# Kernel optimization log

Measured on AMD Instinct MI355X. Metric: run time of the kernel, lower is better.

## Reference

```python
import jax, jax.numpy as jnp
import numpy as np

D_MODEL = 1024; D_STATE = 128; EXPAND = 2; HEADDIM = 64
D_INNER = EXPAND * D_MODEL; NHEADS = D_INNER // HEADDIM; PF = 2  # param_factor for complex
BATCH = 2; SEQ = 2048
DT_MIN = 0.001; DT_MAX = 0.1


def setup_inputs() -> dict:
    key = jax.random.key(0)
    k = jax.random.split(key, 10)
    u = jax.random.normal(k[0], (BATCH, SEQ, D_MODEL), jnp.float32)
    in_proj_w = jax.random.normal(k[1], (2 * D_INNER, D_MODEL), jnp.float32) * (D_MODEL ** -0.5)
    dt_projs_weight = jax.random.normal(k[2], (NHEADS, D_INNER), jnp.float32) * 0.02
    dt_projs_bias = (jax.random.uniform(k[3], (NHEADS,), jnp.float32)
                     * (np.log(DT_MAX) - np.log(DT_MIN)) + np.log(DT_MIN)).astype(jnp.float32)
    x_proj_w = jax.random.normal(k[4], (NHEADS * (1 + 2 * D_STATE * PF), D_INNER), jnp.float32) * (D_INNER ** -0.5)
    A = jnp.stack([-jax.random.uniform(k[5], (NHEADS, D_STATE), dtype=jnp.float32),
                   jax.random.normal(k[6], (NHEADS, D_STATE), jnp.float32) * 0.1], axis=-1)  # (H,N,2)
    D = jnp.ones((NHEADS,), jnp.float32)
    norm_B_w = jnp.ones((2 * D_STATE,), jnp.float32)
    norm_C_w = jnp.ones((2 * D_STATE,), jnp.float32)
    out_proj_w = jax.random.normal(k[7], (D_MODEL, D_INNER), jnp.float32) * (D_INNER ** -0.5)
    return {"u": u, "in_proj_w": in_proj_w, "dt_projs_weight": dt_projs_weight,
            "dt_projs_bias": dt_projs_bias, "x_proj_w": x_proj_w, "A": A, "D": D,
            "norm_B_w": norm_B_w, "norm_C_w": norm_C_w, "out_proj_w": out_proj_w}


def _rms_norm(x, w, eps=1e-6):
    return x * jax.lax.rsqrt(jnp.mean(x * x, axis=-1, keepdims=True) + eps) * w


def reference(u, in_proj_w, dt_projs_weight, dt_projs_bias, x_proj_w, A, D,
              norm_B_w, norm_C_w, out_proj_w):
    Bsz, L, _ = u.shape
    xz = u @ in_proj_w.T                        # (B,L,2*d_inner)
    x, z = jnp.split(xz, 2, axis=-1)
    x = jax.nn.silu(x)                          # (B,L,d_inner)
    dt = jax.nn.softplus(x @ dt_projs_weight.T + dt_projs_bias)  # (B,L,H)

    BCp = (x @ x_proj_w.T).reshape(Bsz, L, NHEADS, -1)
    BC = BCp[..., :2 * D_STATE * PF].reshape(Bsz, L, NHEADS, 2, D_STATE, PF)
    Bn = _rms_norm(BC[..., 0, :, :].reshape(Bsz, L, NHEADS, D_STATE * PF), norm_B_w)
    Cn = _rms_norm(BC[..., 1, :, :].reshape(Bsz, L, NHEADS, D_STATE * PF), norm_C_w)
    Bn = Bn.reshape(Bsz, L, NHEADS, D_STATE, PF)
    Cn = Cn.reshape(Bsz, L, NHEADS, D_STATE, PF)
    Bc = jax.lax.complex(Bn[..., 0], Bn[..., 1])  # (B,L,H,N) complex64
    Cc = jax.lax.complex(Cn[..., 0], Cn[..., 1])
    Ac = jax.lax.complex(A[..., 0], A[..., 1])    # (H,N) complex64

    xh = x.reshape(Bsz, L, NHEADS, HEADDIM)
    x_sum = xh.sum(axis=-1)                       # (B,L,H) -- kernel sums x_t over headdim
    zt = Ac[None, None] * (0.5 * dt)[..., None]   # (B,L,H,N) complex: A*dt/2
    den = 1.0 - zt
    abar = (1.0 + zt) / den                       # bilinear (Tustin) discretization
    u_in = Bc * ((dt * x_sum)[..., None] / den)   # Bbar * sum(x_t)

    def step(h, inp):
        a, b = inp
        h = a * h + b
        return h, h

    h0 = jnp.zeros((Bsz, NHEADS, D_STATE), jnp.complex64)
    _, hs = jax.lax.scan(step, h0, (jnp.swapaxes(abar, 0, 1), jnp.swapaxes(u_in, 0, 1)))
    hs = jnp.swapaxes(hs, 0, 1)                   # (B,L,H,N)
    y_red = jnp.real(Cc * hs).sum(axis=-1)        # (B,L,H), Re(C*h) reduced over state
    y = (xh * (y_red + D)[..., None]).reshape(Bsz, L, D_INNER)
    y = y * jax.nn.silu(z)
    return y @ out_proj_w.T
```

## Files before the change

### kernel.cpp

```cpp
#include <hip/hip_runtime.h>

#define BATCH   2
#define SEQ     2048
#define DMODEL  1024
#define DINNER  2048
#define NHEADS  32
#define HEADDIM 64
#define DSTATE  128
#define BLTOT   (BATCH * SEQ)
#define NCHUNK  32
#define CHUNK   64

#define OFF_UB   0ull
#define OFF_WXZ  8388608ull
#define OFF_WBC  16777216ull
#define OFF_WOUT 83886080ull
#define OFF_XB   88080384ull
#define OFF_YB   104857600ull
#define OFF_BC   121634816ull
#define OFF_SZ   255852544ull
#define OFF_DT   272629760ull
#define OFF_XS   273154048ull
#define OFF_YR   273678336ull
#define OFF_CA   274202624ull
#define OFF_CS   276299776ull
#define OFF_HI   278396928ull
#define OFF_SS   280494080ull
#define OFF_P0   281542656ull
#define OFF_P1   298319872ull

typedef __attribute__((ext_vector_type(8))) short bf16x8;
typedef __attribute__((ext_vector_type(4))) float f32x4;

__device__ __forceinline__ float b2f(unsigned short u) {
    return __uint_as_float(((unsigned)u) << 16);
}
__device__ __forceinline__ unsigned short f2b(float f) {
    unsigned x = __float_as_uint(f);
    unsigned r = (x + 0x7fffu + ((x >> 16) & 1u)) >> 16;
    return (unsigned short)r;
}
__device__ __forceinline__ float silu_f(float v) {
    return v / (1.0f + __expf(-v));
}
__device__ __forceinline__ float softplus_f(float v) {
    return (v > 20.0f) ? v : log1pf(__expf(v));
}

__device__ __forceinline__ void gload_lds16(const void* g, void* l) {
    __builtin_amdgcn_global_load_lds(
        (const __attribute__((address_space(1))) unsigned int*)g,
        (__attribute__((address_space(3))) unsigned int*)l, 16, 0, 0);
}

__global__ __launch_bounds__(256) void conv_all_kernel(
    const float* __restrict__ u, const float* __restrict__ ipw,
    const float* __restrict__ opw, const float* __restrict__ xpw,
    unsigned short* __restrict__ u_b, unsigned short* __restrict__ w_xz,
    unsigned short* __restrict__ w_out, unsigned short* __restrict__ w_bc) {
    long idx = (long)blockIdx.x * 256 + threadIdx.x;
    if (idx >= 2621440L) {
        long e = (idx - 2621440L) * 4;
        long c = e >> 11, k = e & 2047;
        const float* s = xpw + ((c >> 9) * 513 + (c & 511)) * 2048 + k;
        float4 v = *(const float4*)s;
        ushort4 o = {f2b(v.x), f2b(v.y), f2b(v.z), f2b(v.w)};
        *(ushort4*)&w_bc[e] = o;
        return;
    }
    const float* src;
    unsigned short* dst;
    long i;
    if (idx < 1048576L)      { src = u;   dst = u_b;   i = idx; }
    else if (idx < 2097152L) { src = ipw; dst = w_xz;  i = idx - 1048576L; }
    else                     { src = opw; dst = w_out; i = idx - 2097152L; }
    float4 v = *(const float4*)&src[i * 4];
    ushort4 o = {f2b(v.x), f2b(v.y), f2b(v.z), f2b(v.w)};
    *(ushort4*)&dst[i * 4] = o;
}

template <int KTOT, int KLEN, int MODE>
__device__ __forceinline__ void gemm_body(
    const unsigned short* __restrict__ A, const unsigned short* __restrict__ B,
    void* __restrict__ C0, void* __restrict__ C1, float* __restrict__ C2,
    int N, int koff) {
    __shared__ short ldsA[128 * 32];
    __shared__ short ldsB[128 * 32];
    int tid = threadIdx.x;
    int row0 = blockIdx.y * 128, col0 = blockIdx.x * 128;
    int lane = tid & 63, wave = tid >> 6;
    int wrow = (wave >> 1) * 64, wcol = (wave & 1) * 64;
    int m = lane & 15, quad = lane >> 4;

    f32x4 acc[4][4];
#pragma unroll
    for (int i = 0; i < 4; ++i)
#pragma unroll
        for (int j = 0; j < 4; ++j) acc[i][j] = (f32x4){0.f, 0.f, 0.f, 0.f};

    int r = tid >> 2, c8 = (tid & 3) * 8;
    const unsigned short* Ag = A + (size_t)(row0 + r) * KTOT + koff + c8;
    const unsigned short* Bg = B + (size_t)(col0 + r) * KTOT + koff + c8;
    short* la = ldsA + tid * 8;
    short* lb = ldsB + tid * 8;

    for (int k0 = 0; k0 < KLEN; k0 += 32) {
        gload_lds16(Ag + k0, la);
        gload_lds16(Ag + (size_t)64 * KTOT + k0, la + 2048);
        gload_lds16(Bg + k0, lb);
        gload_lds16(Bg + (size_t)64 * KTOT + k0, lb + 2048);
        __syncthreads();
        bf16x8 af[4], bfr[4];
#pragma unroll
        for (int i = 0; i < 4; ++i)
            af[i] = *(const bf16x8*)&ldsA[(wrow + i * 16 + m) * 32 + quad * 8];
#pragma unroll
        for (int j = 0; j < 4; ++j)
            bfr[j] = *(const bf16x8*)&ldsB[(wcol + j * 16 + m) * 32 + quad * 8];
#pragma unroll
        for (int i = 0; i < 4; ++i)
#pragma unroll
            for (int j = 0; j < 4; ++j)
                acc[i][j] = __builtin_amdgcn_mfma_f32_16x16x32_bf16(
                    af[i], bfr[j], acc[i][j], 0, 0, 0);
        __syncthreads();
    }

    if (MODE == 1) {
        bool isx = (col0 < DINNER);
        if (isx) {
            int head = (col0 + wcol) >> 6;
            float ssum[4][4];
#pragma unroll
            for (int i = 0; i < 4; ++i)
#pragma unroll
                for (int reg = 0; reg < 4; ++reg) ssum[i][reg] = 0.f;
#pragma unroll
            for (int i = 0; i < 4; ++i)
#pragma unroll
                for (int reg = 0; reg < 4; ++reg) {
                    int row = row0 + wrow + i * 16 + quad * 4 + reg;
#pragma unroll
                    for (int j = 0; j < 4; ++j) {
                        int col = col0 + wcol + j * 16 + m;
                        float s = silu_f(acc[i][j][reg]);
                        ((unsigned short*)C0)[(size_t)row * DINNER + col] = f2b(s);
                        ssum[i][reg] += s;
                    }
                }
#pragma unroll
            for (int i = 0; i < 4; ++i)
#pragma unroll
                for (int reg = 0; reg < 4; ++reg) {
                    float s = ssum[i][reg];
                    s += __shfl_xor(s, 1);
                    s += __shfl_xor(s, 2);
                    s += __shfl_xor(s, 4);
                    s += __shfl_xor(s, 8);
                    if (m == 0) {
                        int row = row0 + wrow + i * 16 + quad * 4 + reg;
                        C2[(size_t)row * NHEADS + head] = s;
                    }
                }
        } else {
#pragma unroll
            for (int i = 0; i < 4; ++i)
#pragma unroll
                for (int reg = 0; reg < 4; ++reg) {
                    int row = row0 + wrow + i * 16 + quad * 4 + reg;
#pragma unroll
                    for (int j = 0; j < 4; ++j) {
                        int col = col0 + wcol + j * 16 + m - DINNER;
                        float s = silu_f(acc[i][j][reg]);
                        ((unsigned short*)C1)[(size_t)row * DINNER + col] = f2b(s);
                    }
                }
        }
    } else if (MODE == 2) {
        int hH = (col0 + wcol) >> 9;
        int w0 = (col0 + wcol) & 511;
#pragma unroll
        for (int i = 0; i < 4; ++i)
#pragma unroll
            for (int reg = 0; reg < 4; ++reg) {
                int row = row0 + wrow + i * 16 + quad * 4 + reg;
                unsigned short* dst =
                    (unsigned short*)C0 + ((size_t)hH * BLTOT + row) * 512 + w0;
#pragma unroll
                for (int j = 0; j < 4; ++j)
                    dst[j * 16 + m] = f2b(acc[i][j][reg]);
            }
    } else {
#pragma unroll
        for (int i = 0; i < 4; ++i)
#pragma unroll
            for (int reg = 0; reg < 4; ++reg) {
                int row = row0 + wrow + i * 16 + quad * 4 + reg;
#pragma unroll
                for (int j = 0; j < 4; ++j) {
                    int col = col0 + wcol + j * 16 + m;
                    ((float*)C0)[(size_t)row * N + col] = acc[i][j][reg];
                }
            }
    }
}

__global__ __launch_bounds__(256) void gemm_xz_kernel(
    const unsigned short* __restrict__ A, const unsigned short* __restrict__ B,
    void* C0, void* C1, float* C2) {
    gemm_body<1024, 1024, 1>(A, B, C0, C1, C2, 4096, 0);
}
__global__ __launch_bounds__(256) void gemm_bc_kernel(
    const unsigned short* __restrict__ A, const unsigned short* __restrict__ B,
    void* C0) {
    gemm_body<2048, 2048, 2>(A, B, C0, nullptr, nullptr, 16384, 0);
}
__global__ __launch_bounds__(256) void gemm_out_kernel(
    const unsigned short* __restrict__ A, const unsigned short* __restrict__ B,
    float* P0, float* P1) {
    float* dst = blockIdx.z ? P1 : P0;
    gemm_body<2048, 1024, 0>(A, B, dst, nullptr, nullptr, 1024,
                             blockIdx.z * 1024);
}

__global__ __launch_bounds__(256) void yout_reduce_kernel(
    const float* __restrict__ p0, const float* __restrict__ p1,
    float* __restrict__ out) {
    int i = (blockIdx.x * 256 + threadIdx.x) * 4;
    float4 a = *(const float4*)&p0[i];
    float4 b = *(const float4*)&p1[i];
    float4 o = {a.x + b.x, a.y + b.y, a.z + b.z, a.w + b.w};
    *(float4*)&out[i] = o;
}

__global__ __launch_bounds__(256) void dt_kernel(
    const unsigned short* __restrict__ x, const float* __restrict__ dtw,
    const float* __restrict__ dtb, float* __restrict__ dt) {
    __shared__ float xs[8][132];
    __shared__ float ws[32][132];
    int r0 = blockIdx.x * 8;
    int t = threadIdx.x;
    int lrow = t >> 5, lc4 = (t & 31) * 4;
    int lh = t >> 3, lc16 = (t & 7) * 16;
    int row = t >> 5, h = t & 31;
    float acc = 0.f;

    for (int kc = 0; kc < DINNER; kc += 128) {
        ushort4 a = *(const ushort4*)&x[(size_t)(r0 + lrow) * DINNER + kc + lc4];
        xs[lrow][lc4 + 0] = b2f(a.x); xs[lrow][lc4 + 1] = b2f(a.y);
        xs[lrow][lc4 + 2] = b2f(a.z); xs[lrow][lc4 + 3] = b2f(a.w);
#pragma unroll
        for (int q = 0; q < 4; ++q) {
            float4 w = *(const float4*)&dtw[(size_t)lh * DINNER + kc + lc16 + q * 4];
            *(float4*)&ws[lh][lc16 + q * 4] = w;
        }
        __syncthreads();
#pragma unroll
        for (int k = 0; k < 128; k += 4) {
            float4 xv = *(const float4*)&xs[row][k];
            float4 wv = *(const float4*)&ws[h][k];
            acc += xv.x * wv.x + xv.y * wv.y + xv.z * wv.z + xv.w * wv.w;
        }
        __syncthreads();
    }
    dt[(size_t)(r0 + row) * NHEADS + h] = softplus_f(acc + dtb[h]);
}

__global__ __launch_bounds__(256) void ss_kernel(
    const unsigned short* __restrict__ bct, float* __restrict__ ss) {
    int wgid = blockIdx.x * 4 + (threadIdx.x >> 6);
    int lane = threadIdx.x & 63;
    const unsigned short* p = bct + (size_t)wgid * 512 + lane * 8;
    ushort4 a = *(const ushort4*)p;
    ushort4 b = *(const ushort4*)(p + 4);
    float f0 = b2f(a.x), f1 = b2f(a.y), f2 = b2f(a.z), f3 = b2f(a.w);
    float f4 = b2f(b.x), f5 = b2f(b.y), f6 = b2f(b.z), f7 = b2f(b.w);
    float s = f0 * f0 + f1 * f1 + f2 * f2 + f3 * f3 +
              f4 * f4 + f5 * f5 + f6 * f6 + f7 * f7;
    s += __shfl_xor(s, 1);
    s += __shfl_xor(s, 2);
    s += __shfl_xor(s, 4);
    s += __shfl_xor(s, 8);
    s += __shfl_xor(s, 16);
    if ((lane & 31) == 0) ss[(size_t)wgid * 2 + (lane >> 5)] = s;
}

__device__ __forceinline__ void coefs(
    float ar, float ai, float dtv, float xsv, float Br, float Bi,
    float& abr, float& abi, float& ur, float& ui) {
    float hd = 0.5f * dtv;
    float ztr = ar * hd, zti = ai * hd;
    float denr = 1.0f - ztr;
    float s2 = 1.0f / (denr * denr + zti * zti);
    float invr = denr * s2, invi = zti * s2;
    float opr = 1.0f + ztr;
    abr = opr * invr - zti * invi;
    abi = opr * invi + zti * invr;
    float coef = dtv * xsv;
    float cr = coef * invr, ci = coef * invi;
    ur = Br * cr - Bi * ci;
    ui = Br * ci + Bi * cr;
}

__global__ __launch_bounds__(64) void scan_pass1(
    const unsigned short* __restrict__ bct, const float* __restrict__ dt,
    const float* __restrict__ xsum, const float* __restrict__ A,
    const float* __restrict__ wB, const float* __restrict__ ss,
    float2* __restrict__ cA, float2* __restrict__ cS) {
    int blk = blockIdx.x;
    int bh = blk >> 5, c = blk & (NCHUNK - 1);
    int b = bh >> 5, h = bh & 31;
    int t = threadIdx.x;
    float4 av = *(const float4*)&A[(h * DSTATE + 2 * t) * 2];
    float4 wv = *(const float4*)&wB[4 * t];
    int l0 = c * CHUNK;
    size_t rbase = (size_t)h * BLTOT + b * SEQ + l0;
    const unsigned short* base = bct + rbase * 512;
    const float* ssp = ss + rbase * 2;
    const float* dtp = dt + (b * SEQ + l0) * NHEADS + h;
    const float* xsp = xsum + (b * SEQ + l0) * NHEADS + h;

    float pr0 = 1.f, pi0 = 0.f, sr0 = 0.f, si0 = 0.f;
    float pr1 = 1.f, pi1 = 0.f, sr1 = 0.f, si1 = 0.f;
    for (int l = 0; l < CHUNK; ++l) {
        uint2 bw = *(const uint2*)&base[(size_t)l * 512 + 4 * t];
        float scale = rsqrtf(ssp[l * 2] * (1.0f / 256.0f) + 1e-6f);
        float Br0 = b2f((unsigned short)(bw.x & 0xffff)) * scale * wv.x;
        float Bi0 = b2f((unsigned short)(bw.x >> 16)) * scale * wv.y;
        float Br1 = b2f((unsigned short)(bw.y & 0xffff)) * scale * wv.z;
        float Bi1 = b2f((unsigned short)(bw.y >> 16)) * scale * wv.w;
        float dtv = dtp[l * NHEADS], xsv = xsp[l * NHEADS];
        float abr, abi, ur, ui;
        coefs(av.x, av.y, dtv, xsv, Br0, Bi0, abr, abi, ur, ui);
        float ns = abr * sr0 - abi * si0 + ur;
        float nsi = abr * si0 + abi * sr0 + ui;
        sr0 = ns; si0 = nsi;
        float np = abr * pr0 - abi * pi0;
        float npi = abr * pi0 + abi * pr0;
        pr0 = np; pi0 = npi;
        coefs(av.z, av.w, dtv, xsv, Br1, Bi1, abr, abi, ur, ui);
        ns = abr * sr1 - abi * si1 + ur;
        nsi = abr * si1 + abi * sr1 + ui;
        sr1 = ns; si1 = nsi;
        np = abr * pr1 - abi * pi1;
        npi = abr * pi1 + abi * pr1;
        pr1 = np; pi1 = npi;
    }
    size_t idx = ((size_t)bh * NCHUNK + c) * DSTATE + 2 * t;
    *(float4*)&cA[idx] = (float4){pr0, pi0, pr1, pi1};
    *(float4*)&cS[idx] = (float4){sr0, si0, sr1, si1};
}

__global__ __launch_bounds__(128) void scan_fixup(
    const float2* __restrict__ cA, const float2* __restrict__ cS,
    float2* __restrict__ hin) {
    int bh = blockIdx.x;
    int n = threadIdx.x;
    float hr = 0.f, hi = 0.f;
    for (int c = 0; c < NCHUNK; ++c) {
        size_t idx = ((size_t)bh * NCHUNK + c) * DSTATE + n;
        hin[idx] = {hr, hi};
        float2 a = cA[idx];
        float2 s = cS[idx];
        float nhr = a.x * hr - a.y * hi + s.x;
        float nhi = a.x * hi + a.y * hr + s.y;
        hr = nhr; hi = nhi;
    }
}

__global__ __launch_bounds__(64) void scan_pass2(
    const unsigned short* __restrict__ bct, const float* __restrict__ dt,
    const float* __restrict__ xsum, const float* __restrict__ A,
    const float* __restrict__ wB, const float* __restrict__ wC,
    const float* __restrict__ ss, const float2* __restrict__ hin,
    float* __restrict__ yredp) {
    int blk = blockIdx.x;
    int bh = blk >> 5, c = blk & (NCHUNK - 1);
    int b = bh >> 5, h = bh & 31;
    int t = threadIdx.x;
    float4 av = *(const float4*)&A[(h * DSTATE + 2 * t) * 2];
    float4 wbv = *(const float4*)&wB[4 * t];
    float4 wcv = *(const float4*)&wC[4 * t];
    int l0 = c * CHUNK;
    size_t rbase = (size_t)h * BLTOT + b * SEQ + l0;
    const unsigned short* base = bct + rbase * 512;
    const float* ssp = ss + rbase * 2;
    const float* dtp = dt + (b * SEQ + l0) * NHEADS + h;
    const float* xsp = xsum + (b * SEQ + l0) * NHEADS + h;
    float* yp = yredp + (size_t)(b * SEQ + l0) * NHEADS + h;

    float4 h0v = *(const float4*)&hin[((size_t)bh * NCHUNK + c) * DSTATE + 2 * t];
    float hr0 = h0v.x, hi0 = h0v.y, hr1 = h0v.z, hi1 = h0v.w;

    for (int l = 0; l < CHUNK; ++l) {
        uint2 bw = *(const uint2*)&base[(size_t)l * 512 + 4 * t];
        uint2 cw = *(const uint2*)&base[(size_t)l * 512 + 256 + 4 * t];
        float sB = rsqrtf(ssp[l * 2 + 0] * (1.0f / 256.0f) + 1e-6f);
        float sC = rsqrtf(ssp[l * 2 + 1] * (1.0f / 256.0f) + 1e-6f);
        float Br0 = b2f((unsigned short)(bw.x & 0xffff)) * sB * wbv.x;
        float Bi0 = b2f((unsigned short)(bw.x >> 16)) * sB * wbv.y;
        float Br1 = b2f((unsigned short)(bw.y & 0xffff)) * sB * wbv.z;
        float Bi1 = b2f((unsigned short)(bw.y >> 16)) * sB * wbv.w;
        float Cr0 = b2f((unsigned short)(cw.x & 0xffff)) * sC * wcv.x;
        float Ci0 = b2f((unsigned short)(cw.x >> 16)) * sC * wcv.y;
        float Cr1 = b2f((unsigned short)(cw.y & 0xffff)) * sC * wcv.z;
        float Ci1 = b2f((unsigned short)(cw.y >> 16)) * sC * wcv.w;
        float dtv = dtp[l * NHEADS], xsv = xsp[l * NHEADS];
        float abr, abi, ur, ui;
        coefs(av.x, av.y, dtv, xsv, Br0, Bi0, abr, abi, ur, ui);
        float nhr = abr * hr0 - abi * hi0 + ur;
        float nhi = abr * hi0 + abi * hr0 + ui;
        hr0 = nhr; hi0 = nhi;
        coefs(av.z, av.w, dtv, xsv, Br1, Bi1, abr, abi, ur, ui);
        nhr = abr * hr1 - abi * hi1 + ur;
        nhi = abr * hi1 + abi * hr1 + ui;
        hr1 = nhr; hi1 = nhi;
        float y = Cr0 * hr0 - Ci0 * hi0 + Cr1 * hr1 - Ci1 * hi1;
#pragma unroll
        for (int off = 1; off < 64; off <<= 1) y += __shfl_xor(y, off);
        if (t == 0) yp[(size_t)l * NHEADS] = y;
    }
}

__global__ __launch_bounds__(256) void yfuse_kernel(
    const unsigned short* __restrict__ x, const unsigned short* __restrict__ sz,
    const float* __restrict__ yredp, const float* __restrict__ Dv,
    unsigned short* __restrict__ y) {
    int i = (blockIdx.x * 256 + threadIdx.x) * 4;
    int r = i >> 11;
    int k = i & (DINNER - 1);
    int h = k >> 6;
    float yr = yredp[(size_t)r * NHEADS + h] + Dv[h];
    ushort4 xv = *(const ushort4*)&x[i];
    ushort4 zv = *(const ushort4*)&sz[i];
    ushort4 o = {f2b(b2f(xv.x) * yr * b2f(zv.x)),
                 f2b(b2f(xv.y) * yr * b2f(zv.y)),
                 f2b(b2f(xv.z) * yr * b2f(zv.z)),
                 f2b(b2f(xv.w) * yr * b2f(zv.w))};
    *(ushort4*)&y[i] = o;
}

extern "C" void kernel_launch(void* const* d_in, const int* in_sizes, int n_in,
                              void* d_out, int out_size, void* d_ws, size_t ws_size,
                              hipStream_t stream) {
    const float* u   = (const float*)d_in[0];
    const float* ipw = (const float*)d_in[1];
    const float* dtw = (const float*)d_in[2];
    const float* dtb = (const float*)d_in[3];
    const float* xpw = (const float*)d_in[4];
    const float* A   = (const float*)d_in[5];
    const float* Dv  = (const float*)d_in[6];
    const float* wB  = (const float*)d_in[7];
    const float* wC  = (const float*)d_in[8];
    const float* opw = (const float*)d_in[9];
    float* out = (float*)d_out;
    char* ws = (char*)d_ws;

    unsigned short* u_b   = (unsigned short*)(ws + OFF_UB);
    unsigned short* w_xz  = (unsigned short*)(ws + OFF_WXZ);
    unsigned short* w_bc  = (unsigned short*)(ws + OFF_WBC);
    unsigned short* w_out = (unsigned short*)(ws + OFF_WOUT);
    unsigned short* x_b   = (unsigned short*)(ws + OFF_XB);
    unsigned short* y_b   = (unsigned short*)(ws + OFF_YB);
    unsigned short* bct   = (unsigned short*)(ws + OFF_BC);
    unsigned short* sz    = (unsigned short*)(ws + OFF_SZ);
    float* dt    = (float*)(ws + OFF_DT);
    float* xsum  = (float*)(ws + OFF_XS);
    float* yredp = (float*)(ws + OFF_YR);
    float2* cA   = (float2*)(ws + OFF_CA);
    float2* cS   = (float2*)(ws + OFF_CS);
    float2* hin  = (float2*)(ws + OFF_HI);
    float* ssbuf = (float*)(ws + OFF_SS);
    float* p0    = (float*)(ws + OFF_P0);
    float* p1    = (float*)(ws + OFF_P1);

    conv_all_kernel<<<43008, 256, 0, stream>>>(u, ipw, opw, xpw,
                                               u_b, w_xz, w_out, w_bc);

    gemm_xz_kernel<<<dim3(32, 32), 256, 0, stream>>>(u_b, w_xz, x_b, sz, xsum);
    dt_kernel<<<BLTOT / 8, 256, 0, stream>>>(x_b, dtw, dtb, dt);
    gemm_bc_kernel<<<dim3(128, 32), 256, 0, stream>>>(x_b, w_bc, bct);
    ss_kernel<<<NHEADS * BLTOT / 4, 256, 0, stream>>>(bct, ssbuf);

    scan_pass1<<<BATCH * NHEADS * NCHUNK, 64, 0, stream>>>(
        bct, dt, xsum, A, wB, ssbuf, cA, cS);
    scan_fixup<<<BATCH * NHEADS, 128, 0, stream>>>(cA, cS, hin);
    scan_pass2<<<BATCH * NHEADS * NCHUNK, 64, 0, stream>>>(
        bct, dt, xsum, A, wB, wC, ssbuf, hin, yredp);

    yfuse_kernel<<<BLTOT * DINNER / 4 / 256, 256, 0, stream>>>(
        x_b, sz, yredp, Dv, y_b);
    gemm_out_kernel<<<dim3(8, 32, 2), 256, 0, stream>>>(y_b, w_out, p0, p1);
    yout_reduce_kernel<<<BLTOT * DMODEL / 4 / 256, 256, 0, stream>>>(p0, p1, out);
}
```

Before: 832.5 us.

## Fuse y gating into scan pass2, deepen GEMM K-step, precompute rms scales

Removes the separate yfuse kernel: scan_pass2 now multiplies x, the reduced y plus D, and silu(z) directly, writing bf16 y per lane, which drops the yredp round trip and one launch. The shared GEMM body now stages 64 K elements per LDS load instead of 32, halving the number of barriers per tile while doubling LDS use. The RMS-norm rsqrt is moved into ss_kernel so the scan passes read the finished scale instead of recomputing it. The fused epilogue issues 2-byte stores per lane with a stride of one row per step, which coalesces less well than the old vectorized kernel.

```diff
diff --git a/kernel.cpp b/kernel.cpp
--- a/kernel.cpp
+++ b/kernel.cpp
@@ -21,7 +21,6 @@
 #define OFF_SZ   255852544ull
 #define OFF_DT   272629760ull
 #define OFF_XS   273154048ull
-#define OFF_YR   273678336ull
 #define OFF_CA   274202624ull
 #define OFF_CS   276299776ull
 #define OFF_HI   278396928ull
@@ -84,8 +83,8 @@
     const unsigned short* __restrict__ A, const unsigned short* __restrict__ B,
     void* __restrict__ C0, void* __restrict__ C1, float* __restrict__ C2,
     int N, int koff) {
-    __shared__ short ldsA[128 * 32];
-    __shared__ short ldsB[128 * 32];
+    __shared__ short ldsA[128 * 64];
+    __shared__ short ldsB[128 * 64];
     int tid = threadIdx.x;
     int row0 = blockIdx.y * 128, col0 = blockIdx.x * 128;
     int lane = tid & 63, wave = tid >> 6;
@@ -104,25 +103,33 @@
     short* la = ldsA + tid * 8;
     short* lb = ldsB + tid * 8;
 
-    for (int k0 = 0; k0 < KLEN; k0 += 32) {
-        gload_lds16(Ag + k0, la);
-        gload_lds16(Ag + (size_t)64 * KTOT + k0, la + 2048);
-        gload_lds16(Bg + k0, lb);
-        gload_lds16(Bg + (size_t)64 * KTOT + k0, lb + 2048);
+    for (int k0 = 0; k0 < KLEN; k0 += 64) {
+#pragma unroll
+        for (int p = 0; p < 4; ++p) {
+            size_t goff = (size_t)(p >> 1) * 64 * KTOT + (p & 1) * 32 + k0;
+            int loff = (p & 1) * 4096 + (p >> 1) * 2048;
+            gload_lds16(Ag + goff, la + loff);
+            gload_lds16(Bg + goff, lb + loff);
+        }
         __syncthreads();
-        bf16x8 af[4], bfr[4];
-#pragma unroll
-        for (int i = 0; i < 4; ++i)
-            af[i] = *(const bf16x8*)&ldsA[(wrow + i * 16 + m) * 32 + quad * 8];
-#pragma unroll
-        for (int j = 0; j < 4; ++j)
-            bfr[j] = *(const bf16x8*)&ldsB[(wcol + j * 16 + m) * 32 + quad * 8];
-#pragma unroll
-        for (int i = 0; i < 4; ++i)
+#pragma unroll
+        for (int q = 0; q < 2; ++q) {
+            bf16x8 af[4], bfr[4];
+#pragma unroll
+            for (int i = 0; i < 4; ++i)
+                af[i] = *(const bf16x8*)
+                    &ldsA[q * 4096 + (wrow + i * 16 + m) * 32 + quad * 8];
 #pragma unroll
             for (int j = 0; j < 4; ++j)
-                acc[i][j] = __builtin_amdgcn_mfma_f32_16x16x32_bf16(
-                    af[i], bfr[j], acc[i][j], 0, 0, 0);
+                bfr[j] = *(const bf16x8*)
+                    &ldsB[q * 4096 + (wcol + j * 16 + m) * 32 + quad * 8];
+#pragma unroll
+            for (int i = 0; i < 4; ++i)
+#pragma unroll
+                for (int j = 0; j < 4; ++j)
+                    acc[i][j] = __builtin_amdgcn_mfma_f32_16x16x32_bf16(
+                        af[i], bfr[j], acc[i][j], 0, 0, 0);
+        }
         __syncthreads();
     }
 
@@ -282,7 +289,9 @@
     s += __shfl_xor(s, 4);
     s += __shfl_xor(s, 8);
     s += __shfl_xor(s, 16);
-    if ((lane & 31) == 0) ss[(size_t)wgid * 2 + (lane >> 5)] = s;
+    if ((lane & 31) == 0)
+        ss[(size_t)wgid * 2 + (lane >> 5)] =
+            rsqrtf(s * (1.0f / 256.0f) + 1e-6f);
 }
 
 __device__ __forceinline__ void coefs(
@@ -324,7 +333,7 @@
     float pr1 = 1.f, pi1 = 0.f, sr1 = 0.f, si1 = 0.f;
     for (int l = 0; l < CHUNK; ++l) {
         uint2 bw = *(const uint2*)&base[(size_t)l * 512 + 4 * t];
-        float scale = rsqrtf(ssp[l * 2] * (1.0f / 256.0f) + 1e-6f);
+        float scale = ssp[l * 2];
         float Br0 = b2f((unsigned short)(bw.x & 0xffff)) * scale * wv.x;
         float Bi0 = b2f((unsigned short)(bw.x >> 16)) * scale * wv.y;
         float Br1 = b2f((unsigned short)(bw.y & 0xffff)) * scale * wv.z;
@@ -373,7 +382,8 @@
     const float* __restrict__ xsum, const float* __restrict__ A,
     const float* __restrict__ wB, const float* __restrict__ wC,
     const float* __restrict__ ss, const float2* __restrict__ hin,
-    float* __restrict__ yredp) {
+    const unsigned short* __restrict__ xb, const unsigned short* __restrict__ szb,
+    const float* __restrict__ Dv, unsigned short* __restrict__ yb) {
     int blk = blockIdx.x;
     int bh = blk >> 5, c = blk & (NCHUNK - 1);
     int b = bh >> 5, h = bh & 31;
@@ -381,13 +391,14 @@
     float4 av = *(const float4*)&A[(h * DSTATE + 2 * t) * 2];
     float4 wbv = *(const float4*)&wB[4 * t];
     float4 wcv = *(const float4*)&wC[4 * t];
+    float Dh = Dv[h];
     int l0 = c * CHUNK;
     size_t rbase = (size_t)h * BLTOT + b * SEQ + l0;
     const unsigned short* base = bct + rbase * 512;
     const float* ssp = ss + rbase * 2;
     const float* dtp = dt + (b * SEQ + l0) * NHEADS + h;
     const float* xsp = xsum + (b * SEQ + l0) * NHEADS + h;
-    float* yp = yredp + (size_t)(b * SEQ + l0) * NHEADS + h;
+    size_t xoff0 = (size_t)(b * SEQ + l0) * DINNER + h * HEADDIM + t;
 
     float4 h0v = *(const float4*)&hin[((size_t)bh * NCHUNK + c) * DSTATE + 2 * t];
     float hr0 = h0v.x, hi0 = h0v.y, hr1 = h0v.z, hi1 = h0v.w;
@@ -395,8 +406,8 @@
     for (int l = 0; l < CHUNK; ++l) {
         uint2 bw = *(const uint2*)&base[(size_t)l * 512 + 4 * t];
         uint2 cw = *(const uint2*)&base[(size_t)l * 512 + 256 + 4 * t];
-        float sB = rsqrtf(ssp[l * 2 + 0] * (1.0f / 256.0f) + 1e-6f);
-        float sC = rsqrtf(ssp[l * 2 + 1] * (1.0f / 256.0f) + 1e-6f);
+        float sB = ssp[l * 2 + 0];
+        float sC = ssp[l * 2 + 1];
         float Br0 = b2f((unsigned short)(bw.x & 0xffff)) * sB * wbv.x;
         float Bi0 = b2f((unsigned short)(bw.x >> 16)) * sB * wbv.y;
         float Br1 = b2f((unsigned short)(bw.y & 0xffff)) * sB * wbv.z;
@@ -418,26 +429,12 @@
         float y = Cr0 * hr0 - Ci0 * hi0 + Cr1 * hr1 - Ci1 * hi1;
 #pragma unroll
         for (int off = 1; off < 64; off <<= 1) y += __shfl_xor(y, off);
-        if (t == 0) yp[(size_t)l * NHEADS] = y;
-    }
-}
-
-__global__ __launch_bounds__(256) void yfuse_kernel(
-    const unsigned short* __restrict__ x, const unsigned short* __restrict__ sz,
-    const float* __restrict__ yredp, const float* __restrict__ Dv,
-    unsigned short* __restrict__ y) {
-    int i = (blockIdx.x * 256 + threadIdx.x) * 4;
-    int r = i >> 11;
-    int k = i & (DINNER - 1);
-    int h = k >> 6;
-    float yr = yredp[(size_t)r * NHEADS + h] + Dv[h];
-    ushort4 xv = *(const ushort4*)&x[i];
-    ushort4 zv = *(const ushort4*)&sz[i];
-    ushort4 o = {f2b(b2f(xv.x) * yr * b2f(zv.x)),
-                 f2b(b2f(xv.y) * yr * b2f(zv.y)),
-                 f2b(b2f(xv.z) * yr * b2f(zv.z)),
-                 f2b(b2f(xv.w) * yr * b2f(zv.w))};
-    *(ushort4*)&y[i] = o;
+        size_t xo = xoff0 + (size_t)l * DINNER;
+        float yr = y + Dh;
+        float xv = b2f(xb[xo]);
+        float zv = b2f(szb[xo]);
+        yb[xo] = f2b(xv * yr * zv);
+    }
 }
 
 extern "C" void kernel_launch(void* const* d_in, const int* in_sizes, int n_in,
@@ -466,7 +463,6 @@
     unsigned short* sz    = (unsigned short*)(ws + OFF_SZ);
     float* dt    = (float*)(ws + OFF_DT);
     float* xsum  = (float*)(ws + OFF_XS);
-    float* yredp = (float*)(ws + OFF_YR);
     float2* cA   = (float2*)(ws + OFF_CA);
     float2* cS   = (float2*)(ws + OFF_CS);
     float2* hin  = (float2*)(ws + OFF_HI);
@@ -486,10 +482,8 @@
         bct, dt, xsum, A, wB, ssbuf, cA, cS);
     scan_fixup<<<BATCH * NHEADS, 128, 0, stream>>>(cA, cS, hin);
     scan_pass2<<<BATCH * NHEADS * NCHUNK, 64, 0, stream>>>(
-        bct, dt, xsum, A, wB, wC, ssbuf, hin, yredp);
-
-    yfuse_kernel<<<BLTOT * DINNER / 4 / 256, 256, 0, stream>>>(
-        x_b, sz, yredp, Dv, y_b);
+        bct, dt, xsum, A, wB, wC, ssbuf, hin, x_b, sz, Dv, y_b);
+
     gemm_out_kernel<<<dim3(8, 32, 2), 256, 0, stream>>>(y_b, w_out, p0, p1);
     yout_reduce_kernel<<<BLTOT * DMODEL / 4 / 256, 256, 0, stream>>>(p0, p1, out);
 }
```

Result: faster. 789.2 us (-5.2%).
